# Kernel optimization log

Measured on AMD Instinct MI355X. Metric: run time of the kernel, lower is better.

Reference implementation:

```python
import jax, jax.numpy as jnp
import numpy as np

ALPHA = 0.1        # self.alpha in the torch module
NUM_CLASSES = 10   # predict_acc hardcodes range(10)


def _sqdist(x, centers):
    # Faithful to sum((x - c)**2, -1) but computed via the gemm identity to
    # avoid materializing the (N, K, D) broadcast the torch code creates.
    x2 = jnp.sum(x * x, axis=1, keepdims=True)          # [N, 1]
    c2 = jnp.sum(centers * centers, axis=1)             # [K]
    d = x2 + c2[None, :] - 2.0 * (x @ centers.T)        # [N, K]
    return jnp.maximum(d, 0.0)                          # clamp fp round-off


def _predict_acc(distance, y):
    n = distance.shape[0]
    y_p = jnp.argmin(distance, axis=1)                  # index[1][:, 0]
    # counts[i, c] = #points assigned to cluster i (only i < 10 matter) with label c
    onehot_cluster = (y_p[:, None] == jnp.arange(NUM_CLASSES)[None, :]).astype(jnp.float32)  # [N, 10]
    onehot_label = (y[:, None] == jnp.arange(NUM_CLASSES)[None, :]).astype(jnp.float32)      # [N, 10]
    counts = onehot_cluster.T @ onehot_label            # [10, 10]
    used = jnp.zeros((NUM_CLASSES,), dtype=bool)
    correct = jnp.float32(0.0)
    for i in range(NUM_CLASSES):
        bin_i = counts[i]
        has_points = jnp.sum(bin_i) > 0                 # empty bincount -> 'continue'
        label = jnp.argmax(bin_i)                       # first max index, like where(bin==max)[0][0]
        # quchong: recursively zero already-used labels == argmax with used masked out
        masked = jnp.where(used, 0.0, bin_i)
        label = jnp.where(used[label], jnp.argmax(masked), label)
        correct = correct + jnp.where(has_points, bin_i[label], 0.0)
        used = jnp.where(has_points, used.at[label].set(True), used)
    return correct / jnp.float32(n)


def setup_inputs() -> dict:
    key = jax.random.key(0)
    kx, ky, kc = jax.random.split(key, 3)
    N, K, D = 262144, 256, 64
    x = jax.random.normal(kx, (N, D), dtype=jnp.float32)
    y = jax.random.randint(ky, (N,), 0, 10, dtype=jnp.int64)
    centers = jax.random.normal(kc, (K, D), dtype=jnp.float32)
    return {"x": x, "y": y, "centers": centers}


def reference(x, y, centers):
    distance = _sqdist(x, centers)                      # caldis, op='l2'
    # calwei: exp(-alpha*log(d+1)) then row-normalize
    we = jnp.exp(-ALPHA * jnp.log1p(distance))
    weight = we / jnp.sum(we, axis=1, keepdims=True)
    loss = jnp.sum(weight * distance)                   # calloss
    acc = _predict_acc(distance, y)
    return (loss, acc)
```

## Files before the change

### kernel.cpp

```cpp
#include <hip/hip_runtime.h>

#define ALPHA 0.1f
#define NUM_CLASSES 10

typedef __attribute__((ext_vector_type(8))) short bf16x8;
typedef __attribute__((ext_vector_type(4))) float f32x4;


__device__ __forceinline__ unsigned pack2(float a, float b) {
    return (__float_as_uint(b) & 0xFFFF0000u) | (__float_as_uint(a) >> 16);
}
__device__ __forceinline__ float truncbf(float a) {
    return __uint_as_float(__float_as_uint(a) & 0xFFFF0000u);
}


__global__ __launch_bounds__(512, 4) void dist_kernel(
    const float* __restrict__ x,
    const int*   __restrict__ y,
    const float* __restrict__ centers,
    float* __restrict__ loss_acc,
    unsigned int* __restrict__ counts,
    int NT)
{
    __shared__ __align__(16) char bstage[4 * 4 * 64 * 16];
    __shared__ float x2s[64];
    __shared__ float c2s[256];
    __shared__ float    comb_swe[8][64];
    __shared__ float    comb_swd[8][64];
    __shared__ unsigned comb_best[8][64];

    const int tid  = threadIdx.x;
    const int w    = tid >> 6;
    const int lane = tid & 63;
    const int q    = lane >> 4;
    const int r    = lane & 15;

    if (tid < 256) {
        const float4* crow = (const float4*)(centers + tid * 64);
        float s = 0.f;
#pragma unroll
        for (int j = 0; j < 16; ++j) {
            float4 v = crow[j];
            s = fmaf(v.x, v.x, s); s = fmaf(v.y, v.y, s);
            s = fmaf(v.z, v.z, s); s = fmaf(v.w, v.w, s);
        }
        c2s[tid] = s;
    }

    bf16x8 af[2][4];
#pragma unroll
    for (int ct = 0; ct < 2; ++ct) {
        const int row = w * 32 + ct * 16 + r;
        const float4* C = (const float4*)(centers + (size_t)row * 64);
        float4 v0 = C[q * 2], v1 = C[q * 2 + 1];
        float4 v2 = C[8 + q * 2], v3 = C[9 + q * 2];
        union { bf16x8 v; unsigned u[4]; } h0, h1, l0, l1;
        h0.u[0] = pack2(v0.x, v0.y); h0.u[1] = pack2(v0.z, v0.w);
        h0.u[2] = pack2(v1.x, v1.y); h0.u[3] = pack2(v1.z, v1.w);
        h1.u[0] = pack2(v2.x, v2.y); h1.u[1] = pack2(v2.z, v2.w);
        h1.u[2] = pack2(v3.x, v3.y); h1.u[3] = pack2(v3.z, v3.w);
        l0.u[0] = pack2(v0.x - truncbf(v0.x), v0.y - truncbf(v0.y));
        l0.u[1] = pack2(v0.z - truncbf(v0.z), v0.w - truncbf(v0.w));
        l0.u[2] = pack2(v1.x - truncbf(v1.x), v1.y - truncbf(v1.y));
        l0.u[3] = pack2(v1.z - truncbf(v1.z), v1.w - truncbf(v1.w));
        l1.u[0] = pack2(v2.x - truncbf(v2.x), v2.y - truncbf(v2.y));
        l1.u[1] = pack2(v2.z - truncbf(v2.z), v2.w - truncbf(v2.w));
        l1.u[2] = pack2(v3.x - truncbf(v3.x), v3.y - truncbf(v3.y));
        l1.u[3] = pack2(v3.z - truncbf(v3.z), v3.w - truncbf(v3.w));
        af[ct][0] = h0.v; af[ct][1] = h1.v; af[ct][2] = l0.v; af[ct][3] = l1.v;
    }
    __syncthreads();

    float c2r[2][4];
#pragma unroll
    for (int ct = 0; ct < 2; ++ct) {
        float4 v = *(const float4*)(c2s + w * 32 + ct * 16 + q * 4);
        c2r[ct][0] = v.x; c2r[ct][1] = v.y; c2r[ct][2] = v.z; c2r[ct][3] = v.w;
    }

    float loss_local = 0.f;

    for (int t = blockIdx.x; t < NT; t += gridDim.x) {
        if (w < 4) {
            const int row = t * 64 + w * 16 + r;
            const float4* X = (const float4*)(x + (size_t)row * 64);
            float4 v0 = X[q * 2], v1 = X[q * 2 + 1];
            float4 v2 = X[8 + q * 2], v3 = X[9 + q * 2];

            float p = v0.x * v0.x;
            p = fmaf(v0.y, v0.y, p); p = fmaf(v0.z, v0.z, p); p = fmaf(v0.w, v0.w, p);
            p = fmaf(v1.x, v1.x, p); p = fmaf(v1.y, v1.y, p); p = fmaf(v1.z, v1.z, p); p = fmaf(v1.w, v1.w, p);
            p = fmaf(v2.x, v2.x, p); p = fmaf(v2.y, v2.y, p); p = fmaf(v2.z, v2.z, p); p = fmaf(v2.w, v2.w, p);
            p = fmaf(v3.x, v3.x, p); p = fmaf(v3.y, v3.y, p); p = fmaf(v3.z, v3.z, p); p = fmaf(v3.w, v3.w, p);
            p += __shfl_xor(p, 16);
            p += __shfl_xor(p, 32);
            if (q == 0) x2s[w * 16 + r] = p;

            union { bf16x8 v; uint4 u4; unsigned u[4]; } h0, h1, l0, l1;
            h0.u[0] = pack2(v0.x, v0.y); h0.u[1] = pack2(v0.z, v0.w);
            h0.u[2] = pack2(v1.x, v1.y); h0.u[3] = pack2(v1.z, v1.w);
            h1.u[0] = pack2(v2.x, v2.y); h1.u[1] = pack2(v2.z, v2.w);
            h1.u[2] = pack2(v3.x, v3.y); h1.u[3] = pack2(v3.z, v3.w);
            l0.u[0] = pack2(v0.x - truncbf(v0.x), v0.y - truncbf(v0.y));
            l0.u[1] = pack2(v0.z - truncbf(v0.z), v0.w - truncbf(v0.w));
            l0.u[2] = pack2(v1.x - truncbf(v1.x), v1.y - truncbf(v1.y));
            l0.u[3] = pack2(v1.z - truncbf(v1.z), v1.w - truncbf(v1.w));
            l1.u[0] = pack2(v2.x - truncbf(v2.x), v2.y - truncbf(v2.y));
            l1.u[1] = pack2(v2.z - truncbf(v2.z), v2.w - truncbf(v2.w));
            l1.u[2] = pack2(v3.x - truncbf(v3.x), v3.y - truncbf(v3.y));
            l1.u[3] = pack2(v3.z - truncbf(v3.z), v3.w - truncbf(v3.w));
            *(uint4*)(bstage + (((w * 4 + 0) * 64 + lane) << 4)) = h0.u4;
            *(uint4*)(bstage + (((w * 4 + 1) * 64 + lane) << 4)) = h1.u4;
            *(uint4*)(bstage + (((w * 4 + 2) * 64 + lane) << 4)) = l0.u4;
            *(uint4*)(bstage + (((w * 4 + 3) * 64 + lane) << 4)) = l1.u4;
        }
        __syncthreads();

#pragma unroll
        for (int pt = 0; pt < 4; ++pt) {
            union { uint4 u4; bf16x8 v; } b0, b1, b2, b3;
            b0.u4 = *(const uint4*)(bstage + (((pt * 4 + 0) * 64 + lane) << 4));
            b1.u4 = *(const uint4*)(bstage + (((pt * 4 + 1) * 64 + lane) << 4));
            b2.u4 = *(const uint4*)(bstage + (((pt * 4 + 2) * 64 + lane) << 4));
            b3.u4 = *(const uint4*)(bstage + (((pt * 4 + 3) * 64 + lane) << 4));
            const float x2p = x2s[pt * 16 + r];

            f32x4 acc[2];
#pragma unroll
            for (int ct = 0; ct < 2; ++ct) {
                f32x4 a = (f32x4){0.f, 0.f, 0.f, 0.f};
                a = __builtin_amdgcn_mfma_f32_16x16x32_bf16(af[ct][0], b0.v, a, 0, 0, 0);
                a = __builtin_amdgcn_mfma_f32_16x16x32_bf16(af[ct][1], b1.v, a, 0, 0, 0);
                a = __builtin_amdgcn_mfma_f32_16x16x32_bf16(af[ct][2], b0.v, a, 0, 0, 0);
                a = __builtin_amdgcn_mfma_f32_16x16x32_bf16(af[ct][3], b1.v, a, 0, 0, 0);
                a = __builtin_amdgcn_mfma_f32_16x16x32_bf16(af[ct][0], b2.v, a, 0, 0, 0);
                a = __builtin_amdgcn_mfma_f32_16x16x32_bf16(af[ct][1], b3.v, a, 0, 0, 0);
                acc[ct] = a;
            }

            float swe = 0.f, swd = 0.f;
            unsigned best = 0xFFFFFFFFu;
#pragma unroll
            for (int ct = 0; ct < 2; ++ct) {
#pragma unroll
                for (int reg = 0; reg < 4; ++reg) {
                    float d = fmaf(-2.f, acc[ct][reg], x2p + c2r[ct][reg]);
                    d = fmaxf(d, 0.f);
                    const unsigned kid = (unsigned)(w * 32 + ct * 16 + q * 4 + reg);
                    unsigned u = (__float_as_uint(d) & 0xFFFFFF00u) | kid;
                    best = min(best, u);
                    float wg = exp2f(-ALPHA * __log2f(1.f + d));
                    swe += wg;
                    swd = fmaf(wg, d, swd);
                }
            }
            swe += __shfl_xor(swe, 16); swe += __shfl_xor(swe, 32);
            swd += __shfl_xor(swd, 16); swd += __shfl_xor(swd, 32);
            best = min(best, (unsigned)__shfl_xor((int)best, 16));
            best = min(best, (unsigned)__shfl_xor((int)best, 32));
            if (q == 0) {
                comb_swe[w][pt * 16 + r] = swe;
                comb_swd[w][pt * 16 + r] = swd;
                comb_best[w][pt * 16 + r] = best;
            }
        }
        __syncthreads();

        if (tid < 64) {
            float SWE = comb_swe[0][tid], SWD = comb_swd[0][tid];
            unsigned BEST = comb_best[0][tid];
#pragma unroll
            for (int g = 1; g < 8; ++g) {
                SWE += comb_swe[g][tid];
                SWD += comb_swd[g][tid];
                BEST = min(BEST, comb_best[g][tid]);
            }
            loss_local += SWD / SWE;
            const unsigned bk = BEST & 0xFFu;
            if (bk < NUM_CLASSES) {
                const int lbl = y[t * 64 + tid];
                atomicAdd(&counts[bk * NUM_CLASSES + lbl], 1u);
            }
        }
    }

    if (w == 0) {
        float v = loss_local;
#pragma unroll
        for (int o = 32; o > 0; o >>= 1) v += __shfl_down(v, o);
        if (lane == 0) atomicAdd(loss_acc, v);
    }
}


__global__ void finalize_kernel(
    const float* __restrict__ loss_acc,
    const unsigned int* __restrict__ counts,
    float* __restrict__ out,
    int N)
{
    if (threadIdx.x == 0 && blockIdx.x == 0) {
        float c[NUM_CLASSES][NUM_CLASSES];
        for (int i = 0; i < NUM_CLASSES; ++i)
            for (int j = 0; j < NUM_CLASSES; ++j)
                c[i][j] = (float)counts[i * NUM_CLASSES + j];

        bool used[NUM_CLASSES];
        for (int i = 0; i < NUM_CLASSES; ++i) used[i] = false;

        float correct = 0.f;
        for (int i = 0; i < NUM_CLASSES; ++i) {
            float rowsum = 0.f;
            for (int j = 0; j < NUM_CLASSES; ++j) rowsum += c[i][j];
            bool has_points = rowsum > 0.f;

            int label = 0;
            float mx = c[i][0];
            for (int j = 1; j < NUM_CLASSES; ++j)
                if (c[i][j] > mx) { mx = c[i][j]; label = j; }

            if (used[label]) {
                float mm = used[0] ? 0.f : c[i][0];
                int l2 = 0;
                for (int j = 1; j < NUM_CLASSES; ++j) {
                    float v = used[j] ? 0.f : c[i][j];
                    if (v > mm) { mm = v; l2 = j; }
                }
                label = l2;
            }

            if (has_points) {
                correct += c[i][label];
                used[label] = true;
            }
        }
        out[0] = loss_acc[0];
        out[1] = correct / (float)N;
    }
}


extern "C" void kernel_launch(void* const* d_in, const int* in_sizes, int n_in,
                              void* d_out, int out_size, void* d_ws, size_t ws_size,
                              hipStream_t stream)
{
    const float* x       = (const float*)d_in[0];
    const int*   y       = (const int*)d_in[1];
    const float* centers = (const float*)d_in[2];
    float* out = (float*)d_out;

    const int N  = in_sizes[0] / 64;
    const int NT = N / 64;

    float* loss          = (float*)d_ws;
    unsigned int* counts = (unsigned int*)((char*)d_ws + 4);

    hipMemsetAsync(d_ws, 0, 512, stream);

    int grid = 1024;
    if (grid > NT) grid = NT;
    dist_kernel<<<grid, 512, 0, stream>>>(x, y, centers, loss, counts, NT);

    finalize_kernel<<<1, 64, 0, stream>>>(loss, counts, out, N);
}
```

Measured before the change: 153.8 us.

## Fold -2 and norm bias into MFMA, prefetch next x tile and labels

Pre-scales the center fragments by -2 and seeds the MFMA accumulator with x2+c2+1, so the matmul output directly equals d+1. This removes the per-element fma and the 1+d add, and the loss uses SWD/SWE-1. It also register-prefetches the next tile's x rows and loads y labels early to hide global memory latency. The trade-offs are that the fmax clamp is dropped, so round-off can yield d+1<1 or negative values that reach log2, and the prefetch raises register pressure.

```diff
diff --git a/kernel.cpp b/kernel.cpp
--- a/kernel.cpp
+++ b/kernel.cpp
@@ -55,38 +55,60 @@
         const float4* C = (const float4*)(centers + (size_t)row * 64);
         float4 v0 = C[q * 2], v1 = C[q * 2 + 1];
         float4 v2 = C[8 + q * 2], v3 = C[9 + q * 2];
+        float4 m0 = make_float4(-2.f * v0.x, -2.f * v0.y, -2.f * v0.z, -2.f * v0.w);
+        float4 m1 = make_float4(-2.f * v1.x, -2.f * v1.y, -2.f * v1.z, -2.f * v1.w);
+        float4 m2 = make_float4(-2.f * v2.x, -2.f * v2.y, -2.f * v2.z, -2.f * v2.w);
+        float4 m3 = make_float4(-2.f * v3.x, -2.f * v3.y, -2.f * v3.z, -2.f * v3.w);
         union { bf16x8 v; unsigned u[4]; } h0, h1, l0, l1;
-        h0.u[0] = pack2(v0.x, v0.y); h0.u[1] = pack2(v0.z, v0.w);
-        h0.u[2] = pack2(v1.x, v1.y); h0.u[3] = pack2(v1.z, v1.w);
-        h1.u[0] = pack2(v2.x, v2.y); h1.u[1] = pack2(v2.z, v2.w);
-        h1.u[2] = pack2(v3.x, v3.y); h1.u[3] = pack2(v3.z, v3.w);
-        l0.u[0] = pack2(v0.x - truncbf(v0.x), v0.y - truncbf(v0.y));
-        l0.u[1] = pack2(v0.z - truncbf(v0.z), v0.w - truncbf(v0.w));
-        l0.u[2] = pack2(v1.x - truncbf(v1.x), v1.y - truncbf(v1.y));
-        l0.u[3] = pack2(v1.z - truncbf(v1.z), v1.w - truncbf(v1.w));
-        l1.u[0] = pack2(v2.x - truncbf(v2.x), v2.y - truncbf(v2.y));
-        l1.u[1] = pack2(v2.z - truncbf(v2.z), v2.w - truncbf(v2.w));
-        l1.u[2] = pack2(v3.x - truncbf(v3.x), v3.y - truncbf(v3.y));
-        l1.u[3] = pack2(v3.z - truncbf(v3.z), v3.w - truncbf(v3.w));
+        h0.u[0] = pack2(m0.x, m0.y); h0.u[1] = pack2(m0.z, m0.w);
+        h0.u[2] = pack2(m1.x, m1.y); h0.u[3] = pack2(m1.z, m1.w);
+        h1.u[0] = pack2(m2.x, m2.y); h1.u[1] = pack2(m2.z, m2.w);
+        h1.u[2] = pack2(m3.x, m3.y); h1.u[3] = pack2(m3.z, m3.w);
+        l0.u[0] = pack2(m0.x - truncbf(m0.x), m0.y - truncbf(m0.y));
+        l0.u[1] = pack2(m0.z - truncbf(m0.z), m0.w - truncbf(m0.w));
+        l0.u[2] = pack2(m1.x - truncbf(m1.x), m1.y - truncbf(m1.y));
+        l0.u[3] = pack2(m1.z - truncbf(m1.z), m1.w - truncbf(m1.w));
+        l1.u[0] = pack2(m2.x - truncbf(m2.x), m2.y - truncbf(m2.y));
+        l1.u[1] = pack2(m2.z - truncbf(m2.z), m2.w - truncbf(m2.w));
+        l1.u[2] = pack2(m3.x - truncbf(m3.x), m3.y - truncbf(m3.y));
+        l1.u[3] = pack2(m3.z - truncbf(m3.z), m3.w - truncbf(m3.w));
         af[ct][0] = h0.v; af[ct][1] = h1.v; af[ct][2] = l0.v; af[ct][3] = l1.v;
     }
+
+    float4 pv0, pv1, pv2, pv3;
+    if (w < 4) {
+        const int row = blockIdx.x * 64 + w * 16 + r;
+        const float4* X = (const float4*)(x + (size_t)row * 64);
+        pv0 = X[q * 2]; pv1 = X[q * 2 + 1];
+        pv2 = X[8 + q * 2]; pv3 = X[9 + q * 2];
+    }
+
     __syncthreads();
 
-    float c2r[2][4];
+    float c2r1[2][4];
 #pragma unroll
     for (int ct = 0; ct < 2; ++ct) {
         float4 v = *(const float4*)(c2s + w * 32 + ct * 16 + q * 4);
-        c2r[ct][0] = v.x; c2r[ct][1] = v.y; c2r[ct][2] = v.z; c2r[ct][3] = v.w;
+        c2r1[ct][0] = v.x + 1.f; c2r1[ct][1] = v.y + 1.f;
+        c2r1[ct][2] = v.z + 1.f; c2r1[ct][3] = v.w + 1.f;
     }
 
     float loss_local = 0.f;
 
     for (int t = blockIdx.x; t < NT; t += gridDim.x) {
+        int ylab = 0;
+        if (tid < 64) ylab = y[t * 64 + tid];
+
         if (w < 4) {
-            const int row = t * 64 + w * 16 + r;
-            const float4* X = (const float4*)(x + (size_t)row * 64);
-            float4 v0 = X[q * 2], v1 = X[q * 2 + 1];
-            float4 v2 = X[8 + q * 2], v3 = X[9 + q * 2];
+            float4 v0 = pv0, v1 = pv1, v2 = pv2, v3 = pv3;
+
+            const int tn = t + gridDim.x;
+            if (tn < NT) {
+                const int row = tn * 64 + w * 16 + r;
+                const float4* X = (const float4*)(x + (size_t)row * 64);
+                pv0 = X[q * 2]; pv1 = X[q * 2 + 1];
+                pv2 = X[8 + q * 2]; pv3 = X[9 + q * 2];
+            }
 
             float p = v0.x * v0.x;
             p = fmaf(v0.y, v0.y, p); p = fmaf(v0.z, v0.z, p); p = fmaf(v0.w, v0.w, p);
@@ -129,7 +151,9 @@
             f32x4 acc[2];
 #pragma unroll
             for (int ct = 0; ct < 2; ++ct) {
-                f32x4 a = (f32x4){0.f, 0.f, 0.f, 0.f};
+                f32x4 a;
+                a[0] = x2p + c2r1[ct][0]; a[1] = x2p + c2r1[ct][1];
+                a[2] = x2p + c2r1[ct][2]; a[3] = x2p + c2r1[ct][3];
                 a = __builtin_amdgcn_mfma_f32_16x16x32_bf16(af[ct][0], b0.v, a, 0, 0, 0);
                 a = __builtin_amdgcn_mfma_f32_16x16x32_bf16(af[ct][1], b1.v, a, 0, 0, 0);
                 a = __builtin_amdgcn_mfma_f32_16x16x32_bf16(af[ct][2], b0.v, a, 0, 0, 0);
@@ -139,29 +163,27 @@
                 acc[ct] = a;
             }
 
-            float swe = 0.f, swd = 0.f;
+            float swe = 0.f, swdu = 0.f;
             unsigned best = 0xFFFFFFFFu;
 #pragma unroll
             for (int ct = 0; ct < 2; ++ct) {
 #pragma unroll
                 for (int reg = 0; reg < 4; ++reg) {
-                    float d = fmaf(-2.f, acc[ct][reg], x2p + c2r[ct][reg]);
-                    d = fmaxf(d, 0.f);
+                    const float u = acc[ct][reg];
                     const unsigned kid = (unsigned)(w * 32 + ct * 16 + q * 4 + reg);
-                    unsigned u = (__float_as_uint(d) & 0xFFFFFF00u) | kid;
-                    best = min(best, u);
-                    float wg = exp2f(-ALPHA * __log2f(1.f + d));
+                    best = min(best, (__float_as_uint(u) & 0xFFFFFF00u) | kid);
+                    float wg = exp2f(-ALPHA * __log2f(u));
                     swe += wg;
-                    swd = fmaf(wg, d, swd);
+                    swdu = fmaf(wg, u, swdu);
                 }
             }
             swe += __shfl_xor(swe, 16); swe += __shfl_xor(swe, 32);
-            swd += __shfl_xor(swd, 16); swd += __shfl_xor(swd, 32);
+            swdu += __shfl_xor(swdu, 16); swdu += __shfl_xor(swdu, 32);
             best = min(best, (unsigned)__shfl_xor((int)best, 16));
             best = min(best, (unsigned)__shfl_xor((int)best, 32));
             if (q == 0) {
                 comb_swe[w][pt * 16 + r] = swe;
-                comb_swd[w][pt * 16 + r] = swd;
+                comb_swd[w][pt * 16 + r] = swdu;
                 comb_best[w][pt * 16 + r] = best;
             }
         }
@@ -176,11 +198,10 @@
                 SWD += comb_swd[g][tid];
                 BEST = min(BEST, comb_best[g][tid]);
             }
-            loss_local += SWD / SWE;
+            loss_local += SWD / SWE - 1.f;
             const unsigned bk = BEST & 0xFFu;
             if (bk < NUM_CLASSES) {
-                const int lbl = y[t * 64 + tid];
-                atomicAdd(&counts[bk * NUM_CLASSES + lbl], 1u);
+                atomicAdd(&counts[bk * NUM_CLASSES + ylab], 1u);
             }
         }
     }
```

New measurement: 151.4 us. Within noise of the previous version (-1.5%).
